# Kernel optimization log

Measured on AMD Instinct MI355X. Metric: run time of the kernel, lower is better.

The kernel has to match this reference:

```python
import jax, jax.numpy as jnp
import numpy as np

B, C, D = 8, 2048, 768
EPS = 1e-5


def setup_inputs() -> dict:
    key = jax.random.key(0)
    kx, kk, kq, kv = jax.random.split(key, 4)
    x = jax.random.normal(kx, (B, C, D), dtype=jnp.float32)
    # torch.nn.Linear(dim_in, dim_out, bias=False) -> weight [dim_out, dim_in]
    s = 1.0 / np.sqrt(D)
    Wk = jax.random.uniform(kk, (D, D), dtype=jnp.float32, minval=-s, maxval=s)
    Wq = jax.random.uniform(kq, (D, D), dtype=jnp.float32, minval=-s, maxval=s)
    Wv = jax.random.uniform(kv, (D, D), dtype=jnp.float32, minval=-s, maxval=s)
    return {"x": x, "Wk": Wk, "Wq": Wq, "Wv": Wv}


def reference(x, Wk, Wq, Wv):
    # LayerNorm over the last two dims [C, D] (fresh affine: gamma=1, beta=0)
    mean = jnp.mean(x, axis=(-2, -1), keepdims=True)
    var = jnp.mean(jnp.square(x - mean), axis=(-2, -1), keepdims=True)
    xn = (x - mean) * jax.lax.rsqrt(var + EPS)
    # Linear projections: y = x @ W.T
    keys = jnp.einsum('bcd,od->bco', xn, Wk)
    queries = jnp.einsum('bcd,od->bco', xn, Wq)
    values = jnp.einsum('bcd,od->bco', xn, Wv)
    # attention scores [B, C, C], softmax over keys axis (no 1/sqrt(d) in source)
    att = jax.nn.softmax(jnp.einsum('bid,bjd->bij', queries, keys), axis=-1)
    # out[b,i,d] = sum_j values[b,j,d] * att[b,i,j]
    return jnp.einsum('bjd,bij->bid', values, att)
```

## Files before the change

### kernel.cpp

```cpp
#include <hip/hip_runtime.h>
#include <stdint.h>

#define NB 8
#define NC 2048
#define ND 768
#define CD (NC * ND)
#define EPSV 1e-5f

typedef _Float16 f16;
typedef f16 f16x2 __attribute__((ext_vector_type(2)));
typedef f16 f16x8 __attribute__((ext_vector_type(8)));
typedef float f32x4 __attribute__((ext_vector_type(4)));
typedef unsigned short u16;
typedef unsigned int u32;
typedef u32 u32x2 __attribute__((ext_vector_type(2)));
typedef u32 u32x4 __attribute__((ext_vector_type(4)));

__device__ __forceinline__ u16 f2h(float f) {
  return __builtin_bit_cast(u16, (f16)f);
}
__device__ __forceinline__ u32 pack2(float a, float b) {
  f16x2 h = {(f16)a, (f16)b};
  return __builtin_bit_cast(u32, h);
}

__device__ __forceinline__ float wave_sum(float v) {
#pragma unroll
  for (int o = 32; o > 0; o >>= 1) v += __shfl_down(v, o);
  return v;
}
__device__ __forceinline__ float wave_max(float v) {
#pragma unroll
  for (int o = 32; o > 0; o >>= 1) v = fmaxf(v, __shfl_down(v, o));
  return v;
}

__global__ __launch_bounds__(256) void ln_stats(const float* __restrict__ x,
                                                float* __restrict__ stats) {
  const int b = blockIdx.y;
  const float4* xb = (const float4*)(x + (size_t)b * CD);
  const int base = blockIdx.x * 6144;
  float s1 = 0.f, s2 = 0.f;
  for (int i = threadIdx.x; i < 6144; i += 256) {
    float4 v = xb[base + i];
    s1 += (v.x + v.y) + (v.z + v.w);
    s2 += (v.x * v.x + v.y * v.y) + (v.z * v.z + v.w * v.w);
  }
  s1 = wave_sum(s1);
  s2 = wave_sum(s2);
  __shared__ float r1[4], r2[4];
  const int lane = threadIdx.x & 63, w = threadIdx.x >> 6;
  if (lane == 0) { r1[w] = s1; r2[w] = s2; }
  __syncthreads();
  if (threadIdx.x == 0) {
    atomicAdd(&stats[b * 2], (r1[0] + r1[1]) + (r1[2] + r1[3]));
    atomicAdd(&stats[b * 2 + 1], (r2[0] + r2[1]) + (r2[2] + r2[3]));
  }
}

__global__ __launch_bounds__(256) void ln_apply(const float* __restrict__ x,
                                                const float* __restrict__ stats,
                                                u16* __restrict__ xn) {
  const size_t i = ((size_t)blockIdx.x * 256 + threadIdx.x) * 8;
  const int b = (int)(i / CD);
  const float mean = stats[b * 2] * (1.f / CD);
  const float var = stats[b * 2 + 1] * (1.f / CD) - mean * mean;
  const float rstd = rsqrtf(var + EPSV);
  const float4 v0 = *(const float4*)(x + i);
  const float4 v1 = *(const float4*)(x + i + 4);
  u32x4 p;
  p.x = pack2((v0.x - mean) * rstd, (v0.y - mean) * rstd);
  p.y = pack2((v0.z - mean) * rstd, (v0.w - mean) * rstd);
  p.z = pack2((v1.x - mean) * rstd, (v1.y - mean) * rstd);
  p.w = pack2((v1.z - mean) * rstd, (v1.w - mean) * rstd);
  *(u32x4*)(xn + i) = p;
}

__global__ __launch_bounds__(256) void cast_w(const float* __restrict__ Wk,
                                              const float* __restrict__ Wq,
                                              const float* __restrict__ Wv,
                                              u16* __restrict__ Wb) {
  const size_t i = ((size_t)blockIdx.x * 256 + threadIdx.x) * 8;
  const size_t WSZ = (size_t)ND * ND;
  const float* src;
  size_t off;
  if (i < WSZ) { src = Wk; off = i; }
  else if (i < 2 * WSZ) { src = Wq; off = i - WSZ; }
  else { src = Wv; off = i - 2 * WSZ; }
  const float4 v0 = *(const float4*)(src + off);
  const float4 v1 = *(const float4*)(src + off + 4);
  u32x4 p;
  p.x = pack2(v0.x, v0.y);
  p.y = pack2(v0.z, v0.w);
  p.z = pack2(v1.x, v1.y);
  p.w = pack2(v1.z, v1.w);
  *(u32x4*)(Wb + i) = p;
}

__device__ __forceinline__ void stage_tile(u16* lds, const u16* g, int lda, int tid) {
#pragma unroll
  for (int i = 0; i < 2; ++i) {
    const int s = tid + i * 256;
    const u16* gp = g + (size_t)(s >> 2) * lda + (s & 3) * 8;
    __builtin_amdgcn_global_load_lds(
        (const __attribute__((address_space(1))) void*)gp,
        (__attribute__((address_space(3))) void*)(lds + s * 8), 16, 0, 0);
  }
}

__device__ __forceinline__ void gemm_core(const u16* __restrict__ Ab, int lda,
                                          const u16* __restrict__ Bb, int ldb, int nk,
                                          u16 (*ldsA)[4096], u16 (*ldsB)[4096], int tid,
                                          f32x4 acc[4][4]) {
  stage_tile(ldsA[0], Ab, lda, tid);
  stage_tile(ldsB[0], Bb, ldb, tid);
  const int lane = tid & 63, w = tid >> 6;
  const int wr = w >> 1, wc = w & 1;
  const int fr = lane & 15;
  const int ko = (lane >> 4) * 8;
  const int aoff = (wr * 64 + fr) * 32 + ko;
  const int boff = (wc * 64 + fr) * 32 + ko;
  __syncthreads();
  int cur = 0;
  for (int kt = 0; kt < nk; ++kt) {
    if (kt + 1 < nk) {
      stage_tile(ldsA[cur ^ 1], Ab + (size_t)(kt + 1) * 32, lda, tid);
      stage_tile(ldsB[cur ^ 1], Bb + (size_t)(kt + 1) * 32, ldb, tid);
    }
    f16x8 av[4], bv[4];
#pragma unroll
    for (int m = 0; m < 4; ++m) av[m] = *(const f16x8*)&ldsA[cur][aoff + m * 512];
#pragma unroll
    for (int n = 0; n < 4; ++n) bv[n] = *(const f16x8*)&ldsB[cur][boff + n * 512];
#pragma unroll
    for (int m = 0; m < 4; ++m)
#pragma unroll
      for (int n = 0; n < 4; ++n)
        acc[m][n] = __builtin_amdgcn_mfma_f32_16x16x32_f16(av[m], bv[n], acc[m][n], 0, 0, 0);
    __syncthreads();
    cur ^= 1;
  }
}

__global__ __launch_bounds__(256, 2) void gemm_proj(const u16* __restrict__ xn,
                                                    const u16* __restrict__ Wb,
                                                    u16* __restrict__ Kb,
                                                    u16* __restrict__ Qb,
                                                    u16* __restrict__ Vt) {
  __shared__ u16 ldsA[2][4096];
  __shared__ u16 ldsB[2][4096];
  const int tid = threadIdx.x;
  const int brow = blockIdx.x * 128;
  const int bcol = blockIdx.y * 128;
  const int z = blockIdx.z;
  const u16* Ab = xn + (size_t)brow * ND;
  const u16* Bb = Wb + (size_t)z * ND * ND + (size_t)bcol * ND;
  f32x4 acc[4][4] = {};
  gemm_core(Ab, ND, Bb, ND, ND / 32, ldsA, ldsB, tid, acc);
  const int lane = tid & 63, w = tid >> 6, wr = w >> 1, wc = w & 1;
  const int r0 = brow + wr * 64 + ((lane >> 4) << 2);
  const int c0 = bcol + wc * 64 + (lane & 15);
  if (z < 2) {
    u16* O = (z == 0) ? Kb : Qb;
#pragma unroll
    for (int m = 0; m < 4; ++m)
#pragma unroll
      for (int n = 0; n < 4; ++n)
#pragma unroll
        for (int q = 0; q < 4; ++q)
          O[(size_t)(r0 + m * 16 + q) * ND + (c0 + n * 16)] = f2h(acc[m][n][q]);
  } else {
    const int bb = r0 >> 11;
    const int cc = r0 & 2047;
#pragma unroll
    for (int m = 0; m < 4; ++m)
#pragma unroll
      for (int n = 0; n < 4; ++n) {
        u32x2 p;
        p.x = pack2(acc[m][n][0], acc[m][n][1]);
        p.y = pack2(acc[m][n][2], acc[m][n][3]);
        u16* dst = Vt + ((size_t)bb * ND + (c0 + n * 16)) * NC + (cc + m * 16);
        *(u32x2*)dst = p;
      }
  }
}

__global__ __launch_bounds__(256, 2) void gemm_qk(const u16* __restrict__ Qb,
                                                  const u16* __restrict__ Kb,
                                                  float* __restrict__ S) {
  __shared__ u16 ldsA[2][4096];
  __shared__ u16 ldsB[2][4096];
  const int tid = threadIdx.x;
  const int bz = blockIdx.z;
  const u16* Ab = Qb + ((size_t)bz * NC + blockIdx.x * 128) * ND;
  const u16* Bb = Kb + ((size_t)bz * NC + blockIdx.y * 128) * ND;
  float* Sb = S + (size_t)bz * NC * NC;
  f32x4 acc[4][4] = {};
  gemm_core(Ab, ND, Bb, ND, ND / 32, ldsA, ldsB, tid, acc);
  const int lane = tid & 63, w = tid >> 6, wr = w >> 1, wc = w & 1;
  const int r0 = blockIdx.x * 128 + wr * 64 + ((lane >> 4) << 2);
  const int c0 = blockIdx.y * 128 + wc * 64 + (lane & 15);
#pragma unroll
  for (int m = 0; m < 4; ++m)
#pragma unroll
    for (int n = 0; n < 4; ++n)
#pragma unroll
      for (int q = 0; q < 4; ++q)
        Sb[(size_t)(r0 + m * 16 + q) * NC + (c0 + n * 16)] = acc[m][n][q];
}

__global__ __launch_bounds__(256) void softmax_rows(float* __restrict__ S) {
  float* Sr = S + (size_t)blockIdx.x * NC;
  const int t = threadIdx.x;
  const float4* Sv = (const float4*)Sr;
  const float4 v0 = Sv[2 * t];
  const float4 v1 = Sv[2 * t + 1];
  float mv = fmaxf(fmaxf(fmaxf(v0.x, v0.y), fmaxf(v0.z, v0.w)),
                   fmaxf(fmaxf(v1.x, v1.y), fmaxf(v1.z, v1.w)));
  mv = wave_max(mv);
  __shared__ float rm[4], rs[4];
  const int lane = t & 63, w = t >> 6;
  if (lane == 0) rm[w] = mv;
  __syncthreads();
  const float bm = fmaxf(fmaxf(rm[0], rm[1]), fmaxf(rm[2], rm[3]));
  const float e0 = __expf(v0.x - bm), e1 = __expf(v0.y - bm);
  const float e2 = __expf(v0.z - bm), e3 = __expf(v0.w - bm);
  const float e4 = __expf(v1.x - bm), e5 = __expf(v1.y - bm);
  const float e6 = __expf(v1.z - bm), e7 = __expf(v1.w - bm);
  float s = ((e0 + e1) + (e2 + e3)) + ((e4 + e5) + (e6 + e7));
  s = wave_sum(s);
  if (lane == 0) rs[w] = s;
  __syncthreads();
  const float inv = 1.f / ((rs[0] + rs[1]) + (rs[2] + rs[3]));
  u32x4 p;
  p.x = pack2(e0 * inv, e1 * inv);
  p.y = pack2(e2 * inv, e3 * inv);
  p.z = pack2(e4 * inv, e5 * inv);
  p.w = pack2(e6 * inv, e7 * inv);
  u16* ar = (u16*)Sr;
  *(u32x4*)(ar + t * 8) = p;
}

__global__ __launch_bounds__(256, 2) void gemm_av(const u16* __restrict__ att,
                                                  const u16* __restrict__ Vt,
                                                  float* __restrict__ out) {
  __shared__ u16 ldsA[2][4096];
  __shared__ u16 ldsB[2][4096];
  const int tid = threadIdx.x;
  const int bz = blockIdx.z;
  const u16* Ab = att + (size_t)bz * NC * (NC * 2) + (size_t)(blockIdx.x * 128) * (NC * 2);
  const u16* Bb = Vt + ((size_t)bz * ND + blockIdx.y * 128) * NC;
  float* Ob = out + (size_t)bz * NC * ND;
  f32x4 acc[4][4] = {};
  gemm_core(Ab, NC * 2, Bb, NC, NC / 32, ldsA, ldsB, tid, acc);
  const int lane = tid & 63, w = tid >> 6, wr = w >> 1, wc = w & 1;
  const int r0 = blockIdx.x * 128 + wr * 64 + ((lane >> 4) << 2);
  const int c0 = blockIdx.y * 128 + wc * 64 + (lane & 15);
#pragma unroll
  for (int m = 0; m < 4; ++m)
#pragma unroll
    for (int n = 0; n < 4; ++n)
#pragma unroll
      for (int q = 0; q < 4; ++q)
        Ob[(size_t)(r0 + m * 16 + q) * ND + (c0 + n * 16)] = acc[m][n][q];
}

extern "C" void kernel_launch(void* const* d_in, const int* in_sizes, int n_in,
                              void* d_out, int out_size, void* d_ws, size_t ws_size,
                              hipStream_t stream) {
  (void)in_sizes; (void)n_in; (void)out_size; (void)ws_size;
  const float* x = (const float*)d_in[0];
  const float* Wk = (const float*)d_in[1];
  const float* Wq = (const float*)d_in[2];
  const float* Wv = (const float*)d_in[3];
  char* ws = (char*)d_ws;
  float* stats = (float*)ws;
  u16* xn = (u16*)(ws + 256);
  u16* Wb = (u16*)(ws + 25166080);
  u16* Qb = (u16*)(ws + 28705024);
  u16* Kb = (u16*)(ws + 53870848);
  u16* Vt = (u16*)(ws + 79036672);
  float* S = (float*)(ws + 104202496);
  float* out = (float*)d_out;

  hipMemsetAsync(stats, 0, 64, stream);
  ln_stats<<<dim3(64, 8), 256, 0, stream>>>(x, stats);
  ln_apply<<<6144, 256, 0, stream>>>(x, stats, xn);
  cast_w<<<864, 256, 0, stream>>>(Wk, Wq, Wv, Wb);
  gemm_proj<<<dim3(128, 6, 3), 256, 0, stream>>>(xn, Wb, Kb, Qb, Vt);
  gemm_qk<<<dim3(16, 16, 8), 256, 0, stream>>>(Qb, Kb, S);
  softmax_rows<<<16384, 256, 0, stream>>>(S);
  gemm_av<<<dim3(16, 6, 8), 256, 0, stream>>>((const u16*)S, Vt, out);
}
```

Baseline: 382.9 us.

## Rewrite GEMM core as 256x256 tile, 8-wave, swizzled LDS, interleaved prefetch

```diff
diff --git a/kernel.cpp b/kernel.cpp
--- a/kernel.cpp
+++ b/kernel.cpp
@@ -97,116 +97,168 @@
   *(u32x4*)(Wb + i) = p;
 }
 
-__device__ __forceinline__ void stage_tile(u16* lds, const u16* g, int lda, int tid) {
-#pragma unroll
-  for (int i = 0; i < 2; ++i) {
-    const int s = tid + i * 256;
-    const u16* gp = g + (size_t)(s >> 2) * lda + (s & 3) * 8;
-    __builtin_amdgcn_global_load_lds(
-        (const __attribute__((address_space(1))) void*)gp,
-        (__attribute__((address_space(3))) void*)(lds + s * 8), 16, 0, 0);
-  }
-}
-
-__device__ __forceinline__ void gemm_core(const u16* __restrict__ Ab, int lda,
-                                          const u16* __restrict__ Bb, int ldb, int nk,
-                                          u16 (*ldsA)[4096], u16 (*ldsB)[4096], int tid,
-                                          f32x4 acc[4][4]) {
-  stage_tile(ldsA[0], Ab, lda, tid);
-  stage_tile(ldsB[0], Bb, ldb, tid);
-  const int lane = tid & 63, w = tid >> 6;
-  const int wr = w >> 1, wc = w & 1;
+__device__ __forceinline__ void stage_chunk(u16* dst, const u16* src, int ld, int tid) {
+  const int rl = tid >> 2;
+  const int sc = (tid & 3) ^ ((tid >> 3) & 3);
+  const u16* gp = src + (size_t)rl * ld + sc * 8;
+  __builtin_amdgcn_global_load_lds(
+      (const __attribute__((address_space(1))) void*)gp,
+      (__attribute__((address_space(3))) void*)(dst + tid * 8), 16, 0, 0);
+}
+
+__device__ __forceinline__ void mf16(f32x4 acc[8][4], int mb, const f16x8 a[4],
+                                     const f16x8 b[4]) {
+#pragma unroll
+  for (int m = 0; m < 4; ++m)
+#pragma unroll
+    for (int n = 0; n < 4; ++n)
+      acc[mb + m][n] =
+          __builtin_amdgcn_mfma_f32_16x16x32_f16(a[m], b[n], acc[mb + m][n], 0, 0, 0);
+}
+
+__device__ __forceinline__ void gemm256(const u16* __restrict__ A, int lda,
+                                        const u16* __restrict__ B, int ldb, int nk,
+                                        u16 (*lds)[2][4][4096], int tid,
+                                        f32x4 acc[8][4]) {
+  const int lane = tid & 63;
+  const int wc = (tid >> 6) & 3;
+  const int wr = (tid >> 8) & 1;
   const int fr = lane & 15;
-  const int ko = (lane >> 4) * 8;
-  const int aoff = (wr * 64 + fr) * 32 + ko;
-  const int boff = (wc * 64 + fr) * 32 + ko;
-  __syncthreads();
-  int cur = 0;
-  for (int kt = 0; kt < nk; ++kt) {
-    if (kt + 1 < nk) {
-      stage_tile(ldsA[cur ^ 1], Ab + (size_t)(kt + 1) * 32, lda, tid);
-      stage_tile(ldsB[cur ^ 1], Bb + (size_t)(kt + 1) * 32, ldb, tid);
-    }
-    f16x8 av[4], bv[4];
-#pragma unroll
-    for (int m = 0; m < 4; ++m) av[m] = *(const f16x8*)&ldsA[cur][aoff + m * 512];
-#pragma unroll
-    for (int n = 0; n < 4; ++n) bv[n] = *(const f16x8*)&ldsB[cur][boff + n * 512];
-#pragma unroll
-    for (int m = 0; m < 4; ++m)
-#pragma unroll
-      for (int n = 0; n < 4; ++n)
-        acc[m][n] = __builtin_amdgcn_mfma_f32_16x16x32_f16(av[m], bv[n], acc[m][n], 0, 0, 0);
-    __syncthreads();
-    cur ^= 1;
-  }
-}
-
-__global__ __launch_bounds__(256, 2) void gemm_proj(const u16* __restrict__ xn,
+  const int SL = (lane >> 4) ^ ((lane >> 1) & 3);
+  int aoff[4], boff[4];
+#pragma unroll
+  for (int m = 0; m < 4; ++m) aoff[m] = (wr * 64 + m * 16 + fr) * 32 + SL * 8;
+#pragma unroll
+  for (int n = 0; n < 4; ++n) boff[n] = (wc * 32 + (n & 1) * 16 + fr) * 32 + SL * 8;
+
+#define STG_A(BUF, T, KK)                                                  \
+  do {                                                                     \
+    const u16* s_ = A + (size_t)(T) * 64 + (KK) * 32;                      \
+    stage_chunk(&lds[BUF][0][(KK) * 2 + 0][0], s_, lda, tid);              \
+    stage_chunk(&lds[BUF][0][(KK) * 2 + 1][0], s_ + (size_t)128 * lda, lda, tid); \
+  } while (0)
+#define STG_B(BUF, T, KK)                                                  \
+  do {                                                                     \
+    const u16* s_ = B + (size_t)(T) * 64 + (KK) * 32;                      \
+    stage_chunk(&lds[BUF][1][(KK) * 2 + 0][0], s_, ldb, tid);              \
+    stage_chunk(&lds[BUF][1][(KK) * 2 + 1][0], s_ + (size_t)128 * ldb, ldb, tid); \
+  } while (0)
+
+  STG_A(0, 0, 0); STG_B(0, 0, 0); STG_A(0, 0, 1); STG_B(0, 0, 1);
+
+  for (int t = 0; t < nk; ++t) {
+    const int cur = t & 1, nb = cur ^ 1;
+    const bool pre = (t + 1 < nk);
+    f16x8 a[4], b0[4], b1[4];
+    asm volatile("s_waitcnt vmcnt(4)" ::: "memory");
+    __builtin_amdgcn_s_barrier();
+    __builtin_amdgcn_sched_barrier(0);
+    if (pre) STG_A(nb, t + 1, 0);
+#pragma unroll
+    for (int m = 0; m < 4; ++m) a[m] = *(const f16x8*)&lds[cur][0][0][aoff[m]];
+    b0[0] = *(const f16x8*)&lds[cur][1][0][boff[0]];
+    b0[1] = *(const f16x8*)&lds[cur][1][0][boff[1]];
+    b0[2] = *(const f16x8*)&lds[cur][1][1][boff[2]];
+    b0[3] = *(const f16x8*)&lds[cur][1][1][boff[3]];
+    __builtin_amdgcn_s_setprio(1);
+    mf16(acc, 0, a, b0);
+    __builtin_amdgcn_s_setprio(0);
+    if (pre) STG_B(nb, t + 1, 0);
+#pragma unroll
+    for (int m = 0; m < 4; ++m) a[m] = *(const f16x8*)&lds[cur][0][1][aoff[m]];
+    __builtin_amdgcn_s_setprio(1);
+    mf16(acc, 4, a, b0);
+    __builtin_amdgcn_s_setprio(0);
+    if (pre) { asm volatile("s_waitcnt vmcnt(4)" ::: "memory"); }
+    else     { asm volatile("s_waitcnt vmcnt(0)" ::: "memory"); }
+    __builtin_amdgcn_s_barrier();
+    __builtin_amdgcn_sched_barrier(0);
+    if (pre) STG_A(nb, t + 1, 1);
+#pragma unroll
+    for (int m = 0; m < 4; ++m) a[m] = *(const f16x8*)&lds[cur][0][3][aoff[m]];
+    b1[0] = *(const f16x8*)&lds[cur][1][2][boff[0]];
+    b1[1] = *(const f16x8*)&lds[cur][1][2][boff[1]];
+    b1[2] = *(const f16x8*)&lds[cur][1][3][boff[2]];
+    b1[3] = *(const f16x8*)&lds[cur][1][3][boff[3]];
+    __builtin_amdgcn_s_setprio(1);
+    mf16(acc, 4, a, b1);
+    __builtin_amdgcn_s_setprio(0);
+    if (pre) STG_B(nb, t + 1, 1);
+#pragma unroll
+    for (int m = 0; m < 4; ++m) a[m] = *(const f16x8*)&lds[cur][0][2][aoff[m]];
+    __builtin_amdgcn_s_setprio(1);
+    mf16(acc, 0, a, b1);
+    __builtin_amdgcn_s_setprio(0);
+  }
+#undef STG_A
+#undef STG_B
+}
+
+__global__ __launch_bounds__(512, 1) void gemm_proj(const u16* __restrict__ xn,
                                                     const u16* __restrict__ Wb,
                                                     u16* __restrict__ Kb,
                                                     u16* __restrict__ Qb,
                                                     u16* __restrict__ Vt) {
-  __shared__ u16 ldsA[2][4096];
-  __shared__ u16 ldsB[2][4096];
+  __shared__ u16 lds[2][2][4][4096];
   const int tid = threadIdx.x;
-  const int brow = blockIdx.x * 128;
-  const int bcol = blockIdx.y * 128;
+  const int brow = blockIdx.x * 256;
+  const int bcol = blockIdx.y * 256;
   const int z = blockIdx.z;
-  const u16* Ab = xn + (size_t)brow * ND;
-  const u16* Bb = Wb + (size_t)z * ND * ND + (size_t)bcol * ND;
-  f32x4 acc[4][4] = {};
-  gemm_core(Ab, ND, Bb, ND, ND / 32, ldsA, ldsB, tid, acc);
-  const int lane = tid & 63, w = tid >> 6, wr = w >> 1, wc = w & 1;
-  const int r0 = brow + wr * 64 + ((lane >> 4) << 2);
-  const int c0 = bcol + wc * 64 + (lane & 15);
+  f32x4 acc[8][4] = {};
+  gemm256(xn + (size_t)brow * ND, ND, Wb + (size_t)z * ND * ND + (size_t)bcol * ND, ND,
+          ND / 64, lds, tid, acc);
+  const int lane = tid & 63, wc = (tid >> 6) & 3, wr = (tid >> 8) & 1;
   if (z < 2) {
     u16* O = (z == 0) ? Kb : Qb;
 #pragma unroll
-    for (int m = 0; m < 4; ++m)
-#pragma unroll
-      for (int n = 0; n < 4; ++n)
-#pragma unroll
-        for (int q = 0; q < 4; ++q)
-          O[(size_t)(r0 + m * 16 + q) * ND + (c0 + n * 16)] = f2h(acc[m][n][q]);
+    for (int mm = 0; mm < 8; ++mm) {
+      const int r = brow + (mm >> 2) * 128 + wr * 64 + (mm & 3) * 16 + ((lane >> 4) << 2);
+#pragma unroll
+      for (int nn = 0; nn < 4; ++nn) {
+        const int c = bcol + (nn >> 1) * 128 + wc * 32 + (nn & 1) * 16 + (lane & 15);
+#pragma unroll
+        for (int q = 0; q < 4; ++q) O[(size_t)(r + q) * ND + c] = f2h(acc[mm][nn][q]);
+      }
+    }
   } else {
-    const int bb = r0 >> 11;
-    const int cc = r0 & 2047;
-#pragma unroll
-    for (int m = 0; m < 4; ++m)
-#pragma unroll
-      for (int n = 0; n < 4; ++n) {
+#pragma unroll
+    for (int mm = 0; mm < 8; ++mm) {
+      const int r = brow + (mm >> 2) * 128 + wr * 64 + (mm & 3) * 16 + ((lane >> 4) << 2);
+      const int bb = r >> 11;
+      const int cc = r & 2047;
+#pragma unroll
+      for (int nn = 0; nn < 4; ++nn) {
+        const int c = bcol + (nn >> 1) * 128 + wc * 32 + (nn & 1) * 16 + (lane & 15);
         u32x2 p;
-        p.x = pack2(acc[m][n][0], acc[m][n][1]);
-        p.y = pack2(acc[m][n][2], acc[m][n][3]);
-        u16* dst = Vt + ((size_t)bb * ND + (c0 + n * 16)) * NC + (cc + m * 16);
-        *(u32x2*)dst = p;
+        p.x = pack2(acc[mm][nn][0], acc[mm][nn][1]);
+        p.y = pack2(acc[mm][nn][2], acc[mm][nn][3]);
+        *(u32x2*)(Vt + ((size_t)bb * ND + c) * NC + cc) = p;
       }
-  }
-}
-
-__global__ __launch_bounds__(256, 2) void gemm_qk(const u16* __restrict__ Qb,
+    }
+  }
+}
+
+__global__ __launch_bounds__(512, 1) void gemm_qk(const u16* __restrict__ Qb,
                                                   const u16* __restrict__ Kb,
                                                   float* __restrict__ S) {
-  __shared__ u16 ldsA[2][4096];
-  __shared__ u16 ldsB[2][4096];
+  __shared__ u16 lds[2][2][4][4096];
   const int tid = threadIdx.x;
   const int bz = blockIdx.z;
-  const u16* Ab = Qb + ((size_t)bz * NC + blockIdx.x * 128) * ND;
-  const u16* Bb = Kb + ((size_t)bz * NC + blockIdx.y * 128) * ND;
+  f32x4 acc[8][4] = {};
+  gemm256(Qb + ((size_t)bz * NC + blockIdx.x * 256) * ND, ND,
+          Kb + ((size_t)bz * NC + blockIdx.y * 256) * ND, ND, ND / 64, lds, tid, acc);
   float* Sb = S + (size_t)bz * NC * NC;
-  f32x4 acc[4][4] = {};
-  gemm_core(Ab, ND, Bb, ND, ND / 32, ldsA, ldsB, tid, acc);
-  const int lane = tid & 63, w = tid >> 6, wr = w >> 1, wc = w & 1;
-  const int r0 = blockIdx.x * 128 + wr * 64 + ((lane >> 4) << 2);
-  const int c0 = blockIdx.y * 128 + wc * 64 + (lane & 15);
-#pragma unroll
-  for (int m = 0; m < 4; ++m)
-#pragma unroll
-    for (int n = 0; n < 4; ++n)
-#pragma unroll
-      for (int q = 0; q < 4; ++q)
-        Sb[(size_t)(r0 + m * 16 + q) * NC + (c0 + n * 16)] = acc[m][n][q];
+  const int lane = tid & 63, wc = (tid >> 6) & 3, wr = (tid >> 8) & 1;
+#pragma unroll
+  for (int mm = 0; mm < 8; ++mm) {
+    const int r = blockIdx.x * 256 + (mm >> 2) * 128 + wr * 64 + (mm & 3) * 16 + ((lane >> 4) << 2);
+#pragma unroll
+    for (int nn = 0; nn < 4; ++nn) {
+      const int c = blockIdx.y * 256 + (nn >> 1) * 128 + wc * 32 + (nn & 1) * 16 + (lane & 15);
+#pragma unroll
+      for (int q = 0; q < 4; ++q) Sb[(size_t)(r + q) * NC + c] = acc[mm][nn][q];
+    }
+  }
 }
 
 __global__ __launch_bounds__(256) void softmax_rows(float* __restrict__ S) {
@@ -241,28 +293,27 @@
   *(u32x4*)(ar + t * 8) = p;
 }
 
-__global__ __launch_bounds__(256, 2) void gemm_av(const u16* __restrict__ att,
+__global__ __launch_bounds__(512, 1) void gemm_av(const u16* __restrict__ att,
                                                   const u16* __restrict__ Vt,
                                                   float* __restrict__ out) {
-  __shared__ u16 ldsA[2][4096];
-  __shared__ u16 ldsB[2][4096];
+  __shared__ u16 lds[2][2][4][4096];
   const int tid = threadIdx.x;
   const int bz = blockIdx.z;
-  const u16* Ab = att + (size_t)bz * NC * (NC * 2) + (size_t)(blockIdx.x * 128) * (NC * 2);
-  const u16* Bb = Vt + ((size_t)bz * ND + blockIdx.y * 128) * NC;
+  f32x4 acc[8][4] = {};
+  gemm256(att + ((size_t)bz * NC + blockIdx.x * 256) * (NC * 2), NC * 2,
+          Vt + ((size_t)bz * ND + blockIdx.y * 256) * NC, NC, NC / 64, lds, tid, acc);
   float* Ob = out + (size_t)bz * NC * ND;
-  f32x4 acc[4][4] = {};
-  gemm_core(Ab, NC * 2, Bb, NC, NC / 32, ldsA, ldsB, tid, acc);
-  const int lane = tid & 63, w = tid >> 6, wr = w >> 1, wc = w & 1;
-  const int r0 = blockIdx.x * 128 + wr * 64 + ((lane >> 4) << 2);
-  const int c0 = blockIdx.y * 128 + wc * 64 + (lane & 15);
-#pragma unroll
-  for (int m = 0; m < 4; ++m)
-#pragma unroll
-    for (int n = 0; n < 4; ++n)
-#pragma unroll
-      for (int q = 0; q < 4; ++q)
-        Ob[(size_t)(r0 + m * 16 + q) * ND + (c0 + n * 16)] = acc[m][n][q];
+  const int lane = tid & 63, wc = (tid >> 6) & 3, wr = (tid >> 8) & 1;
+#pragma unroll
+  for (int mm = 0; mm < 8; ++mm) {
+    const int r = blockIdx.x * 256 + (mm >> 2) * 128 + wr * 64 + (mm & 3) * 16 + ((lane >> 4) << 2);
+#pragma unroll
+    for (int nn = 0; nn < 4; ++nn) {
+      const int c = blockIdx.y * 256 + (nn >> 1) * 128 + wc * 32 + (nn & 1) * 16 + (lane & 15);
+#pragma unroll
+      for (int q = 0; q < 4; ++q) Ob[(size_t)(r + q) * ND + c] = acc[mm][nn][q];
+    }
+  }
 }
 
 extern "C" void kernel_launch(void* const* d_in, const int* in_sizes, int n_in,
@@ -287,8 +338,8 @@
   ln_stats<<<dim3(64, 8), 256, 0, stream>>>(x, stats);
   ln_apply<<<6144, 256, 0, stream>>>(x, stats, xn);
   cast_w<<<864, 256, 0, stream>>>(Wk, Wq, Wv, Wb);
-  gemm_proj<<<dim3(128, 6, 3), 256, 0, stream>>>(xn, Wb, Kb, Qb, Vt);
-  gemm_qk<<<dim3(16, 16, 8), 256, 0, stream>>>(Qb, Kb, S);
+  gemm_proj<<<dim3(64, 3, 3), 512, 0, stream>>>(xn, Wb, Kb, Qb, Vt);
+  gemm_qk<<<dim3(8, 8, 8), 512, 0, stream>>>(Qb, Kb, S);
   softmax_rows<<<16384, 256, 0, stream>>>(S);
-  gemm_av<<<dim3(16, 6, 8), 256, 0, stream>>>((const u16*)S, Vt, out);
-}
+  gemm_av<<<dim3(8, 3, 8), 512, 0, stream>>>((const u16*)S, Vt, out);
+}
```

Result: faster. 367.9 us (-3.9%).
